# Performance work log

Hardware: AMD Instinct MI355X
Metric: run time of the kernel (lower is better)

## Reference

```python
import jax, jax.numpy as jnp
import numpy as np

EPS = 1e-6
B, N, WD, R = 64, 1024, 64, 4
IN_DIM, HID, OUT_DIM = 512, 512, 256


def oneplus(x):
    return 1.0 + jax.nn.softplus(x)


def content_weight(M, keys, strengths):
    # M:[B,N,W] keys:[B,R,W] strengths:[B,R] -> softmax over N -> [B,N,R]
    Mn = M * jax.lax.rsqrt(jnp.sum(M * M, -1, keepdims=True) + EPS)
    kn = keys * jax.lax.rsqrt(jnp.sum(keys * keys, -1, keepdims=True) + EPS)
    sim = jnp.einsum('bnw,brw->bnr', Mn, kn)
    return jax.nn.softmax(sim * strengths[:, None, :], axis=1)


def allocation(u):
    # DNC allocation weighting: sort usage ascending, exclusive cumprod, scatter back
    idx = jnp.argsort(u, axis=-1)
    us = jnp.take_along_axis(u, idx, -1)
    cp = jnp.cumprod(us, -1)
    cp_excl = jnp.concatenate([jnp.ones_like(cp[:, :1]), cp[:, :-1]], -1)
    a_sorted = (1.0 - us) * cp_excl
    inv = jnp.argsort(idx, axis=-1)
    return jnp.take_along_axis(a_sorted, inv, -1)


def setup_inputs() -> dict:
    key = jax.random.key(0)
    ks = jax.random.split(key, 16)
    rw = jax.random.uniform(ks[0], (B, N, R), dtype=jnp.float32)
    rw = rw / jnp.sum(rw, axis=1, keepdims=True)  # valid read distribution over N
    wwp = jax.random.uniform(ks[1], (B, N), dtype=jnp.float32)
    wwp = wwp / jnp.sum(wwp, axis=1, keepdims=True)
    s = 0.02
    return {
        'x': jax.random.normal(ks[2], (B, IN_DIM), dtype=jnp.float32),
        'read_weighting': rw,
        'memory': jax.random.normal(ks[3], (B, N, WD), dtype=jnp.float32) * 0.1,
        'usage': jax.random.uniform(ks[4], (B, N), dtype=jnp.float32),
        'write_weighting_prev': wwp,
        'link': jnp.zeros((B, N, N), dtype=jnp.float32),
        'precedence': jnp.zeros((B, N), dtype=jnp.float32),
        'W1': jax.random.normal(ks[5], (IN_DIM + R * WD, HID), dtype=jnp.float32) * s,
        'b1': jnp.zeros((HID,), dtype=jnp.float32),
        'Wo': jax.random.normal(ks[6], (HID, OUT_DIM), dtype=jnp.float32) * s,
        'bo': jnp.zeros((OUT_DIM,), dtype=jnp.float32),
        'Wr': jax.random.normal(ks[7], (R * WD, OUT_DIM), dtype=jnp.float32) * s,
        'br': jnp.zeros((OUT_DIM,), dtype=jnp.float32),
        'Wxi': jax.random.normal(ks[8], (HID, WD * R + 3 * WD + 5 * R + 3), dtype=jnp.float32) * s,
        'bxi': jnp.zeros((WD * R + 3 * WD + 5 * R + 3,), dtype=jnp.float32),
    }


def reference(x, read_weighting, memory, usage, write_weighting_prev, link, precedence,
              W1, b1, Wo, bo, Wr, br, Wxi, bxi):
    b, n, wd = memory.shape
    r = read_weighting.shape[-1]
    # --- read with incoming read weighting ---
    read_flat = jnp.einsum('bnw,bnr->brw', memory, read_weighting).reshape(b, r * wd)
    h = jax.nn.relu(jnp.concatenate([x, read_flat], -1) @ W1 + b1)
    output = (h @ Wo + bo) + (read_flat @ Wr + br)
    xi = h @ Wxi + bxi
    # --- interface split ---
    sizes = [wd * r, r, wd, 1, wd, wd, r, 1, 1, 3 * r]
    offs = np.cumsum([0] + sizes)
    p = [xi[:, offs[i]:offs[i + 1]] for i in range(10)]
    read_keys = p[0].reshape(b, r, wd)
    read_strengths = oneplus(p[1])
    write_key = p[2][:, None, :]
    write_strength = oneplus(p[3])
    erase = jax.nn.sigmoid(p[4])
    write_vec = p[5]
    free = jax.nn.sigmoid(p[6])
    ag = jax.nn.sigmoid(p[7])
    wg = jax.nn.sigmoid(p[8])
    read_modes = jax.nn.softmax(p[9].reshape(b, r, 3), axis=-1)
    # --- dynamic memory allocation ---
    retention = jnp.prod(1.0 - free[:, None, :] * read_weighting, axis=-1)  # [B,N]
    usage_new = (usage + write_weighting_prev - usage * write_weighting_prev) * retention
    alloc = allocation(usage_new)
    wc = content_weight(memory, write_key, write_strength)[:, :, 0]
    ww = wg * (ag * alloc + (1.0 - ag) * wc)  # [B,N]
    # --- erase / write ---
    memory_new = memory * (1.0 - ww[:, :, None] * erase[:, None, :]) \
        + ww[:, :, None] * write_vec[:, None, :]
    # --- temporal link matrix ---
    prec_new = (1.0 - jnp.sum(ww, -1, keepdims=True)) * precedence + ww
    link_new = (1.0 - ww[:, :, None] - ww[:, None, :]) * link \
        + ww[:, :, None] * precedence[:, None, :]
    link_new = link_new * (1.0 - jnp.eye(n, dtype=link.dtype))
    fwd_w = jnp.einsum('bij,bjr->bir', link_new, read_weighting)
    bwd_w = jnp.einsum('bji,bjr->bir', link_new, read_weighting)
    # --- new read weighting ---
    cr = content_weight(memory_new, read_keys, read_strengths)
    rw_new = read_modes[:, None, :, 0] * bwd_w \
        + read_modes[:, None, :, 1] * cr \
        + read_modes[:, None, :, 2] * fwd_w
    return output, xi, rw_new, memory_new, usage_new
```

## Files before the change

### kernel.cpp

```cpp
#include <hip/hip_runtime.h>

#define NB 64
#define NN 1024
#define WDIM 64
#define RR 4
#define HID 512
#define XID 471
#define EPSF 1e-6f

#define O_OUT   0
#define O_XI    16384
#define O_RW    46528
#define O_MEM   308672
#define O_USAGE 4502976

#define WS_RFPART   0
#define WS_H        65536
#define WS_ALLOC    129024
#define WS_WW       194560
#define WS_V        260096
#define WS_DIAG     784896
#define WS_ROWAB    850432
#define WS_COLPART  1899008
#define WS_EW       10287616
#define WS_SIMWE    10287872
#define WS_ERP      10353408
#define WS_ER       10354432
#define WS_STP      10616576

__device__ __forceinline__ float sigmoidf_(float x) { return 1.0f / (1.0f + expf(-x)); }
__device__ __forceinline__ float oneplusf_(float x) {
  return 1.0f + ((x > 20.0f) ? x : log1pf(expf(x)));
}

typedef const __attribute__((address_space(1))) void gas_void;
typedef __attribute__((address_space(3))) void las_void;
__device__ __forceinline__ void gl16(const float* g, float* l) {
  __builtin_amdgcn_global_load_lds((gas_void*)g, (las_void*)l, 16, 0, 0);
}

__global__ __launch_bounds__(1024) void k_read_flat(const float* __restrict__ mem,
                                                    const float* __restrict__ rw,
                                                    float* __restrict__ ws) {
  __shared__ float red[1024];
  const int q = blockIdx.x, b = blockIdx.y, t = threadIdx.x;
  const int rwi = t & 255;
  const int r = rwi >> 6, w = rwi & 63;
  const int ng = t >> 8;
  const int n0 = (q << 8) + (ng << 6);
  const float* M  = mem + ((size_t)(b << 10) + n0) * WDIM;
  const float* Rw = rw  + ((size_t)(b << 10) + n0) * RR;
  float a0 = 0.f, a1 = 0.f, a2 = 0.f, a3 = 0.f;
  for (int n = 0; n < 64; n += 4) {
    a0 += M[(n + 0) * WDIM + w] * Rw[(n + 0) * RR + r];
    a1 += M[(n + 1) * WDIM + w] * Rw[(n + 1) * RR + r];
    a2 += M[(n + 2) * WDIM + w] * Rw[(n + 2) * RR + r];
    a3 += M[(n + 3) * WDIM + w] * Rw[(n + 3) * RR + r];
  }
  red[t] = (a0 + a1) + (a2 + a3);
  __syncthreads();
  if (t < 256)
    ws[WS_RFPART + (((q << 6) + b) << 8) + t] =
        red[t] + red[t + 256] + red[t + 512] + red[t + 768];
}

__global__ __launch_bounds__(256) void k_h(const float* __restrict__ x,
                                           const float* __restrict__ W1,
                                           const float* __restrict__ b1,
                                           float* __restrict__ ws) {
  __shared__ float cat[768];
  const int ch = blockIdx.x, b = blockIdx.y, t = threadIdx.x;
  cat[t] = x[b * 512 + t];
  cat[256 + t] = x[b * 512 + 256 + t];
  {
    float s = 0.0f;
    #pragma unroll
    for (int q = 0; q < 4; ++q) s += ws[WS_RFPART + (((q << 6) + b) << 8) + t];
    cat[512 + t] = s;
  }
  __syncthreads();
  const int col = (ch << 8) + t;
  float a0 = 0.f, a1 = 0.f, a2 = 0.f, a3 = 0.f;
  #pragma unroll 4
  for (int k = 0; k < 768; k += 4) {
    a0 = fmaf(cat[k + 0], W1[(k + 0) * 512 + col], a0);
    a1 = fmaf(cat[k + 1], W1[(k + 1) * 512 + col], a1);
    a2 = fmaf(cat[k + 2], W1[(k + 2) * 512 + col], a2);
    a3 = fmaf(cat[k + 3], W1[(k + 3) * 512 + col], a3);
  }
  ws[WS_H + b * 512 + col] = fmaxf(b1[col] + (a0 + a1) + (a2 + a3), 0.0f);
}

__global__ __launch_bounds__(256) void k_xiout(const float* __restrict__ Wxi,
                                               const float* __restrict__ bxi,
                                               const float* __restrict__ Wo,
                                               const float* __restrict__ bo,
                                               const float* __restrict__ Wr,
                                               const float* __restrict__ br,
                                               const float* __restrict__ ws,
                                               float* __restrict__ out) {
  __shared__ float h[512];
  __shared__ float rf[256];
  const int m = blockIdx.x, b = blockIdx.y, t = threadIdx.x;
  h[t] = ws[WS_H + b * 512 + t];
  h[256 + t] = ws[WS_H + b * 512 + 256 + t];
  if (m == 2) {
    float s = 0.0f;
    #pragma unroll
    for (int q = 0; q < 4; ++q) s += ws[WS_RFPART + (((q << 6) + b) << 8) + t];
    rf[t] = s;
  }
  __syncthreads();
  if (m < 2) {
    const int col = (m << 8) + t;
    if (col < XID) {
      float a0 = 0.f, a1 = 0.f, a2 = 0.f, a3 = 0.f;
      #pragma unroll 4
      for (int j = 0; j < 512; j += 4) {
        a0 = fmaf(h[j + 0], Wxi[(j + 0) * XID + col], a0);
        a1 = fmaf(h[j + 1], Wxi[(j + 1) * XID + col], a1);
        a2 = fmaf(h[j + 2], Wxi[(j + 2) * XID + col], a2);
        a3 = fmaf(h[j + 3], Wxi[(j + 3) * XID + col], a3);
      }
      out[O_XI + b * XID + col] = bxi[col] + (a0 + a1) + (a2 + a3);
    }
  } else {
    float a0 = 0.f, a1 = 0.f, a2 = 0.f, a3 = 0.f;
    #pragma unroll 4
    for (int j = 0; j < 512; j += 4) {
      a0 = fmaf(h[j + 0], Wo[(j + 0) * 256 + t], a0);
      a1 = fmaf(h[j + 1], Wo[(j + 1) * 256 + t], a1);
      a2 = fmaf(h[j + 2], Wo[(j + 2) * 256 + t], a2);
      a3 = fmaf(h[j + 3], Wo[(j + 3) * 256 + t], a3);
    }
    #pragma unroll 4
    for (int j = 0; j < 256; j += 4) {
      a0 = fmaf(rf[j + 0], Wr[(j + 0) * 256 + t], a0);
      a1 = fmaf(rf[j + 1], Wr[(j + 1) * 256 + t], a1);
      a2 = fmaf(rf[j + 2], Wr[(j + 2) * 256 + t], a2);
      a3 = fmaf(rf[j + 3], Wr[(j + 3) * 256 + t], a3);
    }
    out[O_OUT + b * 256 + t] = bo[t] + br[t] + (a0 + a1) + (a2 + a3);
  }
}

__global__ __launch_bounds__(256) void k_allocwc(const float* __restrict__ rw,
                                                 const float* __restrict__ usage,
                                                 const float* __restrict__ wwp,
                                                 const float* __restrict__ mem,
                                                 const float* __restrict__ link,
                                                 float* __restrict__ ws,
                                                 float* __restrict__ out) {
  __shared__ float ua[1024];
  __shared__ float la[1024];
  __shared__ float wkn[64];
  __shared__ float red[4];
  __shared__ float swstr;
  const int z = blockIdx.x, b = blockIdx.y, t = threadIdx.x;
  const float* xi = out + O_XI + b * XID;
  if (z < 4) {
    const int q = z;
    const float f0 = sigmoidf_(xi[453]), f1 = sigmoidf_(xi[454]);
    const float f2 = sigmoidf_(xi[455]), f3 = sigmoidf_(xi[456]);
    #pragma unroll
    for (int c = 0; c < 4; ++c) {
      const int n = (c << 8) + t;
      const int i = (b << 10) + n;
      const float4 r4 = *(const float4*)(rw + (size_t)i * 4);
      float ret = (1.0f - f0 * r4.x) * (1.0f - f1 * r4.y) *
                  (1.0f - f2 * r4.z) * (1.0f - f3 * r4.w);
      float u = usage[i], w = wwp[i];
      float un = (u + w - u * w) * ret;
      if (c == q) out[O_USAGE + i] = un;
      ua[n] = un;
      la[n] = logf(un);
    }
    __syncthreads();
    const int i = (q << 8) + t;
    const float ui = ua[i];
    float s0 = 0.f, s1 = 0.f, s2 = 0.f, s3 = 0.f;
    #pragma unroll 2
    for (int j = 0; j < 1024; j += 4) {
      float4 u4 = *(const float4*)(ua + j);
      float4 l4 = *(const float4*)(la + j);
      s0 += ((u4.x < ui) || (u4.x == ui && j + 0 < i)) ? l4.x : 0.0f;
      s1 += ((u4.y < ui) || (u4.y == ui && j + 1 < i)) ? l4.y : 0.0f;
      s2 += ((u4.z < ui) || (u4.z == ui && j + 2 < i)) ? l4.z : 0.0f;
      s3 += ((u4.w < ui) || (u4.w == ui && j + 3 < i)) ? l4.w : 0.0f;
    }
    ws[WS_ALLOC + (b << 10) + i] = (1.0f - ui) * expf((s0 + s1) + (s2 + s3));
  } else {
    const int q = z - 4;
    const int wv = t >> 6, lane = t & 63;
    if (t < 64) {
      float kv = xi[260 + t];
      float ss = kv * kv;
      #pragma unroll
      for (int s = 32; s; s >>= 1) ss += __shfl_xor(ss, s);
      wkn[t] = kv * rsqrtf(ss + EPSF);
    }
    if (t == 64) swstr = oneplusf_(xi[324]);
    __syncthreads();
    const int n = (q << 8) + t;
    const size_t bn = (size_t)(b << 10) + n;
    const float* Mrow = mem + bn * WDIM;
    float dot = 0.0f, ssq = 0.0f;
    #pragma unroll
    for (int w = 0; w < 64; w += 4) {
      float4 m4 = *(const float4*)(Mrow + w);
      float4 k4 = *(const float4*)(&wkn[w]);
      dot += m4.x * k4.x + m4.y * k4.y + m4.z * k4.z + m4.w * k4.w;
      ssq += m4.x * m4.x + m4.y * m4.y + m4.z * m4.z + m4.w * m4.w;
    }
    float e = expf(dot * rsqrtf(ssq + EPSF) * swstr);
    ws[WS_SIMWE + bn] = e;
    ws[WS_DIAG + bn] = link[bn * 1024 + n];
    float se = e;
    #pragma unroll
    for (int s = 32; s; s >>= 1) se += __shfl_xor(se, s);
    if (lane == 0) red[wv] = se;
    __syncthreads();
    if (t == 0) ws[WS_EW + (q << 6) + b] = red[0] + red[1] + red[2] + red[3];
  }
}

__global__ __launch_bounds__(256) void k_wcww_b(const float* __restrict__ mem,
                                                const float* __restrict__ rw,
                                                const float* __restrict__ prec,
                                                float* __restrict__ ws,
                                                float* __restrict__ out) {
  __shared__ float kn[256];
  __shared__ float shev[128];
  __shared__ float smisc[8];
  __shared__ float red8[4][8];
  __shared__ float red4[4][4];
  const int q = blockIdx.x, b = blockIdx.y, t = threadIdx.x;
  const int wv = t >> 6, lane = t & 63;
  const float* xi = out + O_XI + b * XID;
  {
    float kv = xi[(wv << 6) + lane];
    float ss = kv * kv;
    #pragma unroll
    for (int s = 32; s; s >>= 1) ss += __shfl_xor(ss, s);
    kn[t] = kv * rsqrtf(ss + EPSF);
  }
  if (t < 64) shev[t] = sigmoidf_(xi[325 + t]);
  else if (t < 128) shev[t] = xi[389 + (t - 64)];
  else if (t < 132) smisc[t - 128] = oneplusf_(xi[256 + (t - 128)]);
  else if (t == 132) smisc[4] = sigmoidf_(xi[457]);
  else if (t == 133) smisc[5] = sigmoidf_(xi[458]);
  __syncthreads();
  const float denom = ws[WS_EW + b] + ws[WS_EW + 64 + b] +
                      ws[WS_EW + 128 + b] + ws[WS_EW + 192 + b];
  const int n = (q << 8) + t;
  const size_t bn = (size_t)(b << 10) + n;
  float wc = ws[WS_SIMWE + bn] / denom;
  float ag = smisc[4], wg = smisc[5];
  float ww = wg * (ag * ws[WS_ALLOC + bn] + (1.0f - ag) * wc);
  ws[WS_WW + bn] = ww;
  float4 r4 = *(const float4*)(rw + bn * 4);
  float* vp = ws + WS_V + bn * 8;
  float4 v0 = {r4.x, r4.y, r4.z, r4.w};
  float4 v1 = {ww * r4.x, ww * r4.y, ww * r4.z, ww * r4.w};
  *(float4*)vp = v0;
  *(float4*)(vp + 4) = v1;
  float p = prec[bn];
  float vals[8] = {p * r4.x, p * r4.y, p * r4.z, p * r4.w,
                   ww * r4.x, ww * r4.y, ww * r4.z, ww * r4.w};
  #pragma unroll
  for (int k = 0; k < 8; ++k) {
    float v = vals[k];
    #pragma unroll
    for (int s = 32; s; s >>= 1) v += __shfl_xor(v, s);
    vals[k] = v;
  }
  if (lane == 0) {
    #pragma unroll
    for (int k = 0; k < 8; ++k) red8[wv][k] = vals[k];
  }
  const float* Mrow = mem + bn * WDIM;
  float* Orow = out + O_MEM + bn * WDIM;
  float dr0 = 0.f, dr1 = 0.f, dr2 = 0.f, dr3 = 0.f, ssqn = 0.f;
  #pragma unroll
  for (int w4 = 0; w4 < 16; ++w4) {
    float4 m4 = *(const float4*)(Mrow + (w4 << 2));
    float4 e4 = *(const float4*)(&shev[w4 << 2]);
    float4 wv4 = *(const float4*)(&shev[64 + (w4 << 2)]);
    float4 o;
    o.x = m4.x * (1.0f - ww * e4.x) + ww * wv4.x;
    o.y = m4.y * (1.0f - ww * e4.y) + ww * wv4.y;
    o.z = m4.z * (1.0f - ww * e4.z) + ww * wv4.z;
    o.w = m4.w * (1.0f - ww * e4.w) + ww * wv4.w;
    *(float4*)(Orow + (w4 << 2)) = o;
    ssqn += o.x * o.x + o.y * o.y + o.z * o.z + o.w * o.w;
    float4 k0 = *(const float4*)(&kn[w4 << 2]);
    float4 k1 = *(const float4*)(&kn[64 + (w4 << 2)]);
    float4 k2 = *(const float4*)(&kn[128 + (w4 << 2)]);
    float4 k3 = *(const float4*)(&kn[192 + (w4 << 2)]);
    dr0 += o.x * k0.x + o.y * k0.y + o.z * k0.z + o.w * k0.w;
    dr1 += o.x * k1.x + o.y * k1.y + o.z * k1.z + o.w * k1.w;
    dr2 += o.x * k2.x + o.y * k2.y + o.z * k2.z + o.w * k2.w;
    dr3 += o.x * k3.x + o.y * k3.y + o.z * k3.z + o.w * k3.w;
  }
  float rs = rsqrtf(ssqn + EPSF);
  float er[4] = {expf(dr0 * rs * smisc[0]), expf(dr1 * rs * smisc[1]),
                 expf(dr2 * rs * smisc[2]), expf(dr3 * rs * smisc[3])};
  float4 er4 = {er[0], er[1], er[2], er[3]};
  *(float4*)(ws + WS_ER + bn * 4) = er4;
  #pragma unroll
  for (int r = 0; r < 4; ++r) {
    float v = er[r];
    #pragma unroll
    for (int s = 32; s; s >>= 1) v += __shfl_xor(v, s);
    er[r] = v;
  }
  if (lane == 0) {
    #pragma unroll
    for (int r = 0; r < 4; ++r) red4[wv][r] = er[r];
  }
  __syncthreads();
  if (t < 8)
    ws[WS_STP + (((q << 6) + b) << 3) + t] =
        red8[0][t] + red8[1][t] + red8[2][t] + red8[3][t];
  else if (t >= 64 && t < 68)
    ws[WS_ERP + (((q << 6) + b) << 2) + (t - 64)] =
        red4[0][t - 64] + red4[1][t - 64] + red4[2][t - 64] + red4[3][t - 64];
}

__global__ __launch_bounds__(256, 4) void k_link(const float* __restrict__ link,
                                                 float* __restrict__ ws) {
  __shared__ float buf[2][4096];
  __shared__ float vtile[2][512];
  __shared__ float ublk[512];
  __shared__ float scr[512];
  const int rg = blockIdx.x, b = blockIdx.y;
  const int wv = threadIdx.x >> 6, lane = threadIdx.x & 63;
  const int i0 = rg << 6;
  const int rot = ((rg << 1) + b) & 15;
  const float* L = link + ((size_t)b << 20) + ((size_t)i0 << 10);
  const float* V = ws + WS_V + ((size_t)b << 13);

  const float* gsrc[4];
  #pragma unroll
  for (int s = 0; s < 4; ++s) {
    const int qq = (wv << 2) + s;
    const int row = (qq << 2) + (lane >> 4);
    const int cb = (lane & 15) ^ (row & 15);
    gsrc[s] = L + (size_t)row * 1024 + (cb << 2);
  }

  float rowAcc[8], colAcc[8];
  #pragma unroll
  for (int k = 0; k < 8; ++k) { rowAcc[k] = 0.0f; colAcc[k] = 0.0f; }

  {
    const int c0 = rot << 6;
    #pragma unroll
    for (int s = 0; s < 4; ++s) gl16(gsrc[s] + c0, &buf[0][((wv << 2) + s) << 8]);
    if (wv < 2) gl16(V + ((size_t)c0 << 3) + (wv << 8) + (lane << 2), &vtile[0][wv << 8]);
    else        gl16(V + ((size_t)(i0 + ((wv - 2) << 5)) << 3) + (lane << 2),
                     &ublk[(wv - 2) << 8]);
  }
  __syncthreads();

  int p = 0;
  #pragma unroll 1
  for (int jt = 0; jt < 16; ++jt) {
    const int jcur = ((jt + rot) & 15);
    if (jt < 15) {
      const int jn = ((jt + 1 + rot) & 15) << 6;
      #pragma unroll
      for (int s = 0; s < 4; ++s)
        gl16(gsrc[s] + jn, &buf[p ^ 1][((wv << 2) + s) << 8]);
      if (wv < 2) {
        gl16(V + ((size_t)jn << 3) + (wv << 8) + (lane << 2), &vtile[p ^ 1][wv << 8]);
        asm volatile("s_waitcnt vmcnt(5)" ::: "memory");
      } else {
        asm volatile("s_waitcnt vmcnt(4)" ::: "memory");
      }
    } else {
      asm volatile("s_waitcnt vmcnt(0)" ::: "memory");
    }
    __builtin_amdgcn_sched_barrier(0);
    __builtin_amdgcn_s_barrier();
    __builtin_amdgcn_sched_barrier(0);
    const float* tb = &buf[p][0];
    if (wv < 2) {
      const float* base = tb + (lane << 6);
      const int rm = lane & 15;
      const float* vt = &vtile[p][0];
      #pragma unroll
      for (int jb8 = 0; jb8 < 8; ++jb8) {
        const int jb = (wv << 3) + jb8;
        float4 f4 = *(const float4*)(base + ((jb ^ rm) << 2));
        const float* vsb = vt + (jb << 5);
        #pragma unroll
        for (int q = 0; q < 4; ++q) {
          float fq = (q == 0) ? f4.x : (q == 1) ? f4.y : (q == 2) ? f4.z : f4.w;
          float4 a = *(const float4*)(vsb + (q << 3));
          float4 c = *(const float4*)(vsb + (q << 3) + 4);
          rowAcc[0] = fmaf(fq, a.x, rowAcc[0]);
          rowAcc[1] = fmaf(fq, a.y, rowAcc[1]);
          rowAcc[2] = fmaf(fq, a.z, rowAcc[2]);
          rowAcc[3] = fmaf(fq, a.w, rowAcc[3]);
          rowAcc[4] = fmaf(fq, c.x, rowAcc[4]);
          rowAcc[5] = fmaf(fq, c.y, rowAcc[5]);
          rowAcc[6] = fmaf(fq, c.z, rowAcc[6]);
          rowAcc[7] = fmaf(fq, c.w, rowAcc[7]);
        }
      }
    } else {
      const int iq = wv - 2;
      #pragma unroll 8
      for (int ii = 0; ii < 32; ++ii) {
        const int i = (iq << 5) + ii;
        float fq = tb[(i << 6) + ((((lane >> 2) ^ (i & 15)) << 2) | (lane & 3))];
        const float* ur = &ublk[i << 3];
        float4 a = *(const float4*)ur;
        float4 cc = *(const float4*)(ur + 4);
        colAcc[0] = fmaf(fq, a.x, colAcc[0]);
        colAcc[1] = fmaf(fq, a.y, colAcc[1]);
        colAcc[2] = fmaf(fq, a.z, colAcc[2]);
        colAcc[3] = fmaf(fq, a.w, colAcc[3]);
        colAcc[4] = fmaf(fq, cc.x, colAcc[4]);
        colAcc[5] = fmaf(fq, cc.y, colAcc[5]);
        colAcc[6] = fmaf(fq, cc.z, colAcc[6]);
        colAcc[7] = fmaf(fq, cc.w, colAcc[7]);
      }
      if (wv == 3) {
        #pragma unroll
        for (int k = 0; k < 8; ++k) scr[(k << 6) + lane] = colAcc[k];
      }
    }
    asm volatile("s_waitcnt lgkmcnt(0)" ::: "memory");
    __builtin_amdgcn_s_barrier();
    __builtin_amdgcn_sched_barrier(0);
    if (wv == 2) {
      float* cp = ws + WS_COLPART + ((((size_t)rg << 6) + (size_t)b) << 13) +
                  (size_t)((jcur << 6) + lane) * 8;
      float s[8];
      #pragma unroll
      for (int k = 0; k < 8; ++k) s[k] = colAcc[k] + scr[(k << 6) + lane];
      float4 c0 = {s[0], s[1], s[2], s[3]};
      float4 c1 = {s[4], s[5], s[6], s[7]};
      *(float4*)cp = c0;
      *(float4*)(cp + 4) = c1;
    }
    if (wv >= 2) {
      #pragma unroll
      for (int k = 0; k < 8; ++k) colAcc[k] = 0.0f;
    }
    p ^= 1;
  }

  __syncthreads();
  if (wv == 1) {
    #pragma unroll
    for (int k = 0; k < 8; ++k) buf[0][(lane << 3) + k] = rowAcc[k];
  }
  __syncthreads();
  if (wv == 0) {
    float* rp = ws + WS_ROWAB + ((size_t)(b << 10) + i0 + lane) * 8;
    #pragma unroll
    for (int k = 0; k < 8; ++k) rowAcc[k] += buf[0][(lane << 3) + k];
    float4 c0 = {rowAcc[0], rowAcc[1], rowAcc[2], rowAcc[3]};
    float4 c1 = {rowAcc[4], rowAcc[5], rowAcc[6], rowAcc[7]};
    *(float4*)rp = c0;
    *(float4*)(rp + 4) = c1;
  }
}

__global__ __launch_bounds__(256) void k_final(const float* __restrict__ rw,
                                               const float* __restrict__ prec,
                                               const float* __restrict__ ws,
                                               float* __restrict__ out) {
  const int q = blockIdx.x, b = blockIdx.y, t = threadIdx.x;
  const float* xi = out + O_XI + b * XID;
  float md0[4], md1[4], md2[4];
  #pragma unroll
  for (int r = 0; r < 4; ++r) {
    float a = xi[459 + r * 3], bb = xi[459 + r * 3 + 1], c = xi[459 + r * 3 + 2];
    float m = fmaxf(a, fmaxf(bb, c));
    float ea = expf(a - m), eb = expf(bb - m), ec = expf(c - m);
    float s = 1.0f / (ea + eb + ec);
    md0[r] = ea * s; md1[r] = eb * s; md2[r] = ec * s;
  }
  float denom[4], ST[8];
  #pragma unroll
  for (int r = 0; r < 4; ++r)
    denom[r] = ws[WS_ERP + (b << 2) + r] + ws[WS_ERP + ((64 + b) << 2) + r] +
               ws[WS_ERP + ((128 + b) << 2) + r] + ws[WS_ERP + ((192 + b) << 2) + r];
  #pragma unroll
  for (int k = 0; k < 8; ++k)
    ST[k] = ws[WS_STP + (b << 3) + k] + ws[WS_STP + ((64 + b) << 3) + k] +
            ws[WS_STP + ((128 + b) << 3) + k] + ws[WS_STP + ((192 + b) << 3) + k];
  const int n = (q << 8) + t;
  const size_t bn = (size_t)(b << 10) + n;
  float4 er4 = *(const float4*)(ws + WS_ER + bn * 4);
  float cr[4] = {er4.x / denom[0], er4.y / denom[1], er4.z / denom[2], er4.w / denom[3]};
  float ca[8];
  #pragma unroll
  for (int k = 0; k < 8; ++k) ca[k] = 0.0f;
  #pragma unroll
  for (int rg = 0; rg < 16; ++rg) {
    const float* p = ws + WS_COLPART + ((((size_t)rg << 6) + (size_t)b) << 13) +
                     (size_t)n * 8;
    float4 a = *(const float4*)p;
    float4 c2 = *(const float4*)(p + 4);
    ca[0] += a.x; ca[1] += a.y; ca[2] += a.z; ca[3] += a.w;
    ca[4] += c2.x; ca[5] += c2.y; ca[6] += c2.z; ca[7] += c2.w;
  }
  const float* ra = ws + WS_ROWAB + bn * 8;
  float d = ws[WS_DIAG + bn];
  float w_ = ws[WS_WW + bn];
  float pn = prec[bn];
  float4 r4 = *(const float4*)(rw + bn * 4);
  float rv[4] = {r4.x, r4.y, r4.z, r4.w};
  float ow = 1.0f - w_;
  float res[4];
  #pragma unroll
  for (int r = 0; r < 4; ++r) {
    float A = ra[r], Ap = ra[4 + r], Bv = ca[r], Bp = ca[4 + r];
    float fwd = ow * (A - d * rv[r]) - (Ap - w_ * d * rv[r]) + w_ * (ST[r] - pn * rv[r]);
    float bwd = ow * (Bv - d * rv[r]) - (Bp - w_ * d * rv[r]) + pn * (ST[4 + r] - w_ * rv[r]);
    res[r] = md0[r] * bwd + md1[r] * cr[r] + md2[r] * fwd;
  }
  float4 o = {res[0], res[1], res[2], res[3]};
  *(float4*)(out + O_RW + bn * 4) = o;
}

extern "C" void kernel_launch(void* const* d_in, const int* in_sizes, int n_in,
                              void* d_out, int out_size, void* d_ws, size_t ws_size,
                              hipStream_t stream) {
  const float* x     = (const float*)d_in[0];
  const float* rw    = (const float*)d_in[1];
  const float* mem   = (const float*)d_in[2];
  const float* usage = (const float*)d_in[3];
  const float* wwp   = (const float*)d_in[4];
  const float* link  = (const float*)d_in[5];
  const float* prec  = (const float*)d_in[6];
  const float* W1    = (const float*)d_in[7];
  const float* b1    = (const float*)d_in[8];
  const float* Wo    = (const float*)d_in[9];
  const float* bo    = (const float*)d_in[10];
  const float* Wr    = (const float*)d_in[11];
  const float* br    = (const float*)d_in[12];
  const float* Wxi   = (const float*)d_in[13];
  const float* bxi   = (const float*)d_in[14];
  float* out = (float*)d_out;
  float* ws = (float*)d_ws;

  k_read_flat<<<dim3(4, 64), 1024, 0, stream>>>(mem, rw, ws);
  k_h<<<dim3(2, 64), 256, 0, stream>>>(x, W1, b1, ws);
  k_xiout<<<dim3(3, 64), 256, 0, stream>>>(Wxi, bxi, Wo, bo, Wr, br, ws, out);
  k_allocwc<<<dim3(8, 64), 256, 0, stream>>>(rw, usage, wwp, mem, link, ws, out);
  k_wcww_b<<<dim3(4, 64), 256, 0, stream>>>(mem, rw, prec, ws, out);
  k_link<<<dim3(16, 64), 256, 0, stream>>>(link, ws);
  k_final<<<dim3(4, 64), 256, 0, stream>>>(rw, prec, ws, out);
}
```

Before: 243.6 us.

## Widen link-matrix column tile to 128 and drop cross-wave column reduction

The k_link kernel now streams 64x128 tiles of the link matrix instead of 64x64, halving the number of pipeline iterations and barriers. The two column waves now each own distinct columns and sum over all 64 rows, so the shared-memory scratch exchange and its extra synchronisation before the column-partial write are gone. Shared memory use roughly doubles and launch bounds drop to 2 blocks per CU, which lowers occupancy and latency hiding. The XOR swizzle is widened to 32 to match the new tile width.

```diff
diff --git a/kernel.cpp b/kernel.cpp
--- a/kernel.cpp
+++ b/kernel.cpp
@@ -327,25 +327,23 @@
         red4[0][t - 64] + red4[1][t - 64] + red4[2][t - 64] + red4[3][t - 64];
 }
 
-__global__ __launch_bounds__(256, 4) void k_link(const float* __restrict__ link,
+__global__ __launch_bounds__(256, 2) void k_link(const float* __restrict__ link,
                                                  float* __restrict__ ws) {
-  __shared__ float buf[2][4096];
-  __shared__ float vtile[2][512];
+  __shared__ float buf[2][8192];
+  __shared__ float vtile[2][1024];
   __shared__ float ublk[512];
-  __shared__ float scr[512];
   const int rg = blockIdx.x, b = blockIdx.y;
   const int wv = threadIdx.x >> 6, lane = threadIdx.x & 63;
   const int i0 = rg << 6;
-  const int rot = ((rg << 1) + b) & 15;
+  const int rot = ((rg << 1) + b) & 7;
   const float* L = link + ((size_t)b << 20) + ((size_t)i0 << 10);
   const float* V = ws + WS_V + ((size_t)b << 13);
 
-  const float* gsrc[4];
-  #pragma unroll
-  for (int s = 0; s < 4; ++s) {
-    const int qq = (wv << 2) + s;
-    const int row = (qq << 2) + (lane >> 4);
-    const int cb = (lane & 15) ^ (row & 15);
+  const float* gsrc[8];
+  #pragma unroll
+  for (int s = 0; s < 8; ++s) {
+    const int row = (wv << 4) + (s << 1) + (lane >> 5);
+    const int cb = (lane & 31) ^ (row & 31);
     gsrc[s] = L + (size_t)row * 1024 + (cb << 2);
   }
 
@@ -354,29 +352,38 @@
   for (int k = 0; k < 8; ++k) { rowAcc[k] = 0.0f; colAcc[k] = 0.0f; }
 
   {
-    const int c0 = rot << 6;
-    #pragma unroll
-    for (int s = 0; s < 4; ++s) gl16(gsrc[s] + c0, &buf[0][((wv << 2) + s) << 8]);
-    if (wv < 2) gl16(V + ((size_t)c0 << 3) + (wv << 8) + (lane << 2), &vtile[0][wv << 8]);
-    else        gl16(V + ((size_t)(i0 + ((wv - 2) << 5)) << 3) + (lane << 2),
-                     &ublk[(wv - 2) << 8]);
+    const int c0 = rot << 7;
+    #pragma unroll
+    for (int s = 0; s < 8; ++s) gl16(gsrc[s] + c0, &buf[0][((wv << 3) + s) << 8]);
+    if (wv < 2) {
+      #pragma unroll
+      for (int s = 0; s < 2; ++s)
+        gl16(V + ((size_t)c0 << 3) + ((((wv << 1) + s) << 8) + (lane << 2)),
+             &vtile[0][((wv << 1) + s) << 8]);
+    } else {
+      gl16(V + ((size_t)i0 << 3) + (((wv - 2) << 8) + (lane << 2)),
+           &ublk[(wv - 2) << 8]);
+    }
   }
   __syncthreads();
 
   int p = 0;
   #pragma unroll 1
-  for (int jt = 0; jt < 16; ++jt) {
-    const int jcur = ((jt + rot) & 15);
-    if (jt < 15) {
-      const int jn = ((jt + 1 + rot) & 15) << 6;
+  for (int jt = 0; jt < 8; ++jt) {
+    const int jcur = ((jt + rot) & 7);
+    if (jt < 7) {
+      const int jn = ((jt + 1 + rot) & 7) << 7;
       #pragma unroll
-      for (int s = 0; s < 4; ++s)
-        gl16(gsrc[s] + jn, &buf[p ^ 1][((wv << 2) + s) << 8]);
+      for (int s = 0; s < 8; ++s)
+        gl16(gsrc[s] + jn, &buf[p ^ 1][((wv << 3) + s) << 8]);
       if (wv < 2) {
-        gl16(V + ((size_t)jn << 3) + (wv << 8) + (lane << 2), &vtile[p ^ 1][wv << 8]);
-        asm volatile("s_waitcnt vmcnt(5)" ::: "memory");
+        #pragma unroll
+        for (int s = 0; s < 2; ++s)
+          gl16(V + ((size_t)jn << 3) + ((((wv << 1) + s) << 8) + (lane << 2)),
+               &vtile[p ^ 1][((wv << 1) + s) << 8]);
+        asm volatile("s_waitcnt vmcnt(10)" ::: "memory");
       } else {
-        asm volatile("s_waitcnt vmcnt(4)" ::: "memory");
+        asm volatile("s_waitcnt vmcnt(8)" ::: "memory");
       }
     } else {
       asm volatile("s_waitcnt vmcnt(0)" ::: "memory");
@@ -386,14 +393,14 @@
     __builtin_amdgcn_sched_barrier(0);
     const float* tb = &buf[p][0];
     if (wv < 2) {
-      const float* base = tb + (lane << 6);
-      const int rm = lane & 15;
+      const float* base = tb + (lane << 7);
+      const int rm = lane & 31;
       const float* vt = &vtile[p][0];
       #pragma unroll
-      for (int jb8 = 0; jb8 < 8; ++jb8) {
-        const int jb = (wv << 3) + jb8;
-        float4 f4 = *(const float4*)(base + ((jb ^ rm) << 2));
-        const float* vsb = vt + (jb << 5);
+      for (int jb = 0; jb < 16; ++jb) {
+        const int jbb = (wv << 4) + jb;
+        float4 f4 = *(const float4*)(base + ((jbb ^ rm) << 2));
+        const float* vsb = vt + (jbb << 5);
         #pragma unroll
         for (int q = 0; q < 4; ++q) {
           float fq = (q == 0) ? f4.x : (q == 1) ? f4.y : (q == 2) ? f4.z : f4.w;
@@ -410,11 +417,11 @@
         }
       }
     } else {
-      const int iq = wv - 2;
+      const int j = ((wv - 2) << 6) + lane;
+      const int jb4 = j >> 2, jlo = j & 3;
       #pragma unroll 8
-      for (int ii = 0; ii < 32; ++ii) {
-        const int i = (iq << 5) + ii;
-        float fq = tb[(i << 6) + ((((lane >> 2) ^ (i & 15)) << 2) | (lane & 3))];
+      for (int i = 0; i < 64; ++i) {
+        float fq = tb[(i << 7) + (((jb4 ^ (i & 31)) << 2) | jlo)];
         const float* ur = &ublk[i << 3];
         float4 a = *(const float4*)ur;
         float4 cc = *(const float4*)(ur + 4);
@@ -427,29 +434,17 @@
         colAcc[6] = fmaf(fq, cc.z, colAcc[6]);
         colAcc[7] = fmaf(fq, cc.w, colAcc[7]);
       }
-      if (wv == 3) {
-        #pragma unroll
-        for (int k = 0; k < 8; ++k) scr[(k << 6) + lane] = colAcc[k];
-      }
-    }
-    asm volatile("s_waitcnt lgkmcnt(0)" ::: "memory");
+      float* cp = ws + WS_COLPART + ((((size_t)rg << 6) + (size_t)b) << 13) +
+                  (size_t)((jcur << 7) + j) * 8;
+      float4 c0 = {colAcc[0], colAcc[1], colAcc[2], colAcc[3]};
+      float4 c1 = {colAcc[4], colAcc[5], colAcc[6], colAcc[7]};
+      *(float4*)cp = c0;
+      *(float4*)(cp + 4) = c1;
+      #pragma unroll
+      for (int k = 0; k < 8; ++k) colAcc[k] = 0.0f;
+    }
     __builtin_amdgcn_s_barrier();
     __builtin_amdgcn_sched_barrier(0);
-    if (wv == 2) {
-      float* cp = ws + WS_COLPART + ((((size_t)rg << 6) + (size_t)b) << 13) +
-                  (size_t)((jcur << 6) + lane) * 8;
-      float s[8];
-      #pragma unroll
-      for (int k = 0; k < 8; ++k) s[k] = colAcc[k] + scr[(k << 6) + lane];
-      float4 c0 = {s[0], s[1], s[2], s[3]};
-      float4 c1 = {s[4], s[5], s[6], s[7]};
-      *(float4*)cp = c0;
-      *(float4*)(cp + 4) = c1;
-    }
-    if (wv >= 2) {
-      #pragma unroll
-      for (int k = 0; k < 8; ++k) colAcc[k] = 0.0f;
-    }
     p ^= 1;
   }
 
```

Measured after the change: 242.4 us. About the same (-0.5%).
